# Performance work log

Hardware: AMD Instinct MI355X
Metric: run time of the kernel (lower is better)

The kernel has to match this reference:

```python
import jax, jax.numpy as jnp
import numpy as np

B, T, N, H = 256, 128, 512, 512
LB, UB = 0.0, 0.1
MAX_IT = 32  # bounded substitute for the data-dependent while loop (converges in a few iters)


def setup_inputs() -> dict:
    key = jax.random.key(0)
    ks = jax.random.split(key, 11)
    s = 1.0 / np.sqrt(H)
    u = lambda k, shape: jax.random.uniform(k, shape, jnp.float32, -s, s)
    return {
        "x": jax.random.normal(ks[0], (B, T, N), jnp.float32),
        "W_ih0": u(ks[1], (3 * H, N)), "W_hh0": u(ks[2], (3 * H, H)),
        "b_ih0": u(ks[3], (3 * H,)), "b_hh0": u(ks[4], (3 * H,)),
        "W_ih1": u(ks[5], (3 * H, H)), "W_hh1": u(ks[6], (3 * H, H)),
        "b_ih1": u(ks[7], (3 * H,)), "b_hh1": u(ks[8], (3 * H,)),
        "fc_w": u(ks[9], (N, H)), "fc_b": u(ks[10], (N,)),
    }


def gru_layer(x, W_ih, W_hh, b_ih, b_hh):
    # x: [B, T, I] -> hidden sequence [B, T, H]; matches torch.nn.GRU gate math.
    xi = jnp.einsum('bti,gi->btg', x, W_ih) + b_ih  # precompute input proj [B,T,3H]

    def step(h, xi_t):
        gh = h @ W_hh.T + b_hh
        xr, xz, xn = jnp.split(xi_t, 3, axis=-1)
        hr, hz, hn = jnp.split(gh, 3, axis=-1)
        r = jax.nn.sigmoid(xr + hr)
        z = jax.nn.sigmoid(xz + hz)
        n = jnp.tanh(xn + r * hn)
        h2 = (1.0 - z) * n + z * h
        return h2, h2

    h0 = jnp.zeros((x.shape[0], H), x.dtype)
    _, hs = jax.lax.scan(step, h0, jnp.swapaxes(xi, 0, 1))
    return jnp.swapaxes(hs, 0, 1)


def rebalance(w):
    # Water-filling: clamp to [LB, UB], redistribute clipped mass to non-capped
    # names proportionally, repeat until no weight exceeds UB. Bounded iteration
    # count with masked no-op updates (do-while semantics: body runs at least once).
    wc0 = jnp.clip(w, LB, UB)

    def body(st, _):
        old, wc, cont = st
        leftover = jnp.sum(old - wc)
        mask = wc != UB
        noms = jnp.where(mask, wc, 0.0)
        gift = leftover * noms / jnp.sum(noms)
        wc2 = wc + gift                      # gift is 0 where mask is False
        again = jnp.any(wc2 > UB)
        wc_next = jnp.where(again, jnp.clip(wc2, LB, UB), wc2)
        old_n = jnp.where(cont, wc2, old)
        wc_n = jnp.where(cont, wc_next, wc)
        return (old_n, wc_n, jnp.logical_and(cont, again)), None

    (old, wc, _), _ = jax.lax.scan(body, (w, wc0, jnp.array(True)), None, length=MAX_IT)
    return wc


def reference(x, W_ih0, W_hh0, b_ih0, b_hh0, W_ih1, W_hh1, b_ih1, b_hh1, fc_w, fc_b):
    h = gru_layer(x, W_ih0, W_hh0, b_ih0, b_hh0)
    h = gru_layer(h, W_ih1, W_hh1, b_ih1, b_hh1)
    h_t = h[:, -1, :]                        # last timestep [B, H]
    logit = h_t @ fc_w.T + fc_b              # dropout is identity in eval
    logit = jax.nn.softmax(jax.nn.silu(logit), axis=-1)
    return jax.vmap(rebalance)(logit)
```

## Files before the change

### kernel.cpp

```cpp
#include <hip/hip_runtime.h>
#include <math.h>

#define BB 256
#define TT 128
#define NN 512
#define HH 512
#define G3 1536
#define SLAB (HH * BB)
#define XSLAB (G3 * BB)
#define CH 16

typedef __attribute__((ext_vector_type(8))) short bf16x8;
typedef __attribute__((ext_vector_type(4))) float f32x4;

__device__ __forceinline__ unsigned short bf16_rne(float f) {
    union { float f; unsigned int u; } v; v.f = f;
    unsigned int r = (v.u + 0x7fffu + ((v.u >> 16) & 1u)) >> 16;
    return (unsigned short)r;
}
__device__ __forceinline__ float bf16_tof(unsigned short h) {
    union { float f; unsigned int u; } v; v.u = ((unsigned int)h) << 16;
    return v.f;
}
__device__ __forceinline__ float sigm(float v) { return 1.f / (1.f + expf(-v)); }

__global__ void zero_kernel(float* p, int n) {
    int i = blockIdx.x * blockDim.x + threadIdx.x;
    if (i < n) p[i] = 0.f;
}

__global__ __launch_bounds__(256) void convert_split(
    const float* __restrict__ in, unsigned short* __restrict__ hi,
    unsigned short* __restrict__ lo, int n) {
    int i = (blockIdx.x * 256 + threadIdx.x) * 4;
    if (i >= n) return;
    float4 v = *(const float4*)(in + i);
    float f[4] = {v.x, v.y, v.z, v.w};
    ushort4 h, l;
    unsigned short* hp = (unsigned short*)&h;
    unsigned short* lp = (unsigned short*)&l;
#pragma unroll
    for (int q = 0; q < 4; ++q) {
        unsigned short hh = bf16_rne(f[q]);
        hp[q] = hh;
        lp[q] = bf16_rne(f[q] - bf16_tof(hh));
    }
    *(ushort4*)(hi + i) = h;
    *(ushort4*)(lo + i) = l;
}

__global__ __launch_bounds__(128) void pack_rec(
    const float* __restrict__ Whh0, const float* __restrict__ Wih1,
    const float* __restrict__ Whh1, unsigned short* __restrict__ pk) {
    int bi = blockIdx.x;
    int set = bi >> 9, rem = bi & 511;
    int p = rem >> 4, kc = rem & 15;
    const float* W = (set == 0) ? Whh0 : (set == 1) ? Wih1 : Whh1;
    unsigned short* tp = pk + (size_t)bi * 4096;
    int tid = threadIdx.x;
#pragma unroll
    for (int i = 0; i < 12; ++i) {
        int idx = tid * 12 + i;
        int row = idx >> 5, k = idx & 31;
        int grow = (row >> 4) * 512 + p * 16 + (row & 15);
        float v = W[(size_t)grow * 512 + kc * 32 + k];
        unsigned short h = bf16_rne(v);
        tp[row * 40 + k] = h;
        tp[1920 + row * 40 + k] = bf16_rne(v - bf16_tof(h));
    }
    if (tid < 32)
#pragma unroll
        for (int i = 0; i < 8; ++i) tp[3840 + tid * 8 + i] = 0;
}

__global__ __launch_bounds__(256) void xi_mfma_x(
    const unsigned short* __restrict__ Wh, const unsigned short* __restrict__ Wl,
    const float* __restrict__ x, int t0,
    const float* __restrict__ bias, float* __restrict__ out) {
    __shared__ unsigned short As[2][128][40];
    __shared__ unsigned short Bs[2][128][40];
    const int tid = threadIdx.x;
    const int n0 = blockIdx.x * 128;
    const int g0 = blockIdx.y * 128;
    const int tl = n0 >> 8, b0 = n0 & 255;
    const int tg = t0 + tl;
    const int w = tid >> 6, lane = tid & 63;
    const int wg = (w >> 1) * 64, wb = (w & 1) * 64;
    const int l15 = lane & 15, l4 = lane >> 4;
    const int sr = tid >> 2, sc = (tid & 3) * 8;

    f32x4 acc[4][4] = {};
    for (int kc = 0; kc < 512; kc += 32) {
        uint4 a0 = *(const uint4*)(Wh + (size_t)(g0 + sr) * 512 + kc + sc);
        uint4 a1 = *(const uint4*)(Wh + (size_t)(g0 + 64 + sr) * 512 + kc + sc);
        uint4 a2 = *(const uint4*)(Wl + (size_t)(g0 + sr) * 512 + kc + sc);
        uint4 a3 = *(const uint4*)(Wl + (size_t)(g0 + 64 + sr) * 512 + kc + sc);
        const float* xr0 = x + ((size_t)(b0 + sr) * TT + tg) * NN + kc + sc;
        const float* xr1 = x + ((size_t)(b0 + 64 + sr) * TT + tg) * NN + kc + sc;
        float4 f00 = *(const float4*)xr0, f01 = *(const float4*)(xr0 + 4);
        float4 f10 = *(const float4*)xr1, f11 = *(const float4*)(xr1 + 4);
        float fa[8] = {f00.x, f00.y, f00.z, f00.w, f01.x, f01.y, f01.z, f01.w};
        float fb[8] = {f10.x, f10.y, f10.z, f10.w, f11.x, f11.y, f11.z, f11.w};
        unsigned short h0v[8], l0v[8], h1v[8], l1v[8];
#pragma unroll
        for (int q = 0; q < 8; ++q) {
            unsigned short hh = bf16_rne(fa[q]);
            h0v[q] = hh; l0v[q] = bf16_rne(fa[q] - bf16_tof(hh));
            hh = bf16_rne(fb[q]);
            h1v[q] = hh; l1v[q] = bf16_rne(fb[q] - bf16_tof(hh));
        }
        __syncthreads();
        *(uint4*)&As[0][sr][sc] = a0;      *(uint4*)&As[0][64 + sr][sc] = a1;
        *(uint4*)&As[1][sr][sc] = a2;      *(uint4*)&As[1][64 + sr][sc] = a3;
        *(uint4*)&Bs[0][sr][sc] = *(uint4*)h0v;  *(uint4*)&Bs[0][64 + sr][sc] = *(uint4*)h1v;
        *(uint4*)&Bs[1][sr][sc] = *(uint4*)l0v;  *(uint4*)&Bs[1][64 + sr][sc] = *(uint4*)l1v;
        __syncthreads();
        bf16x8 ah[4], al[4], bh[4], bl[4];
#pragma unroll
        for (int i = 0; i < 4; ++i) {
            ah[i] = *(const bf16x8*)&As[0][wg + 16 * i + l15][l4 * 8];
            al[i] = *(const bf16x8*)&As[1][wg + 16 * i + l15][l4 * 8];
            bh[i] = *(const bf16x8*)&Bs[0][wb + 16 * i + l15][l4 * 8];
            bl[i] = *(const bf16x8*)&Bs[1][wb + 16 * i + l15][l4 * 8];
        }
#pragma unroll
        for (int i = 0; i < 4; ++i)
#pragma unroll
            for (int j = 0; j < 4; ++j) {
                acc[i][j] = __builtin_amdgcn_mfma_f32_16x16x32_bf16(ah[i], bh[j], acc[i][j], 0, 0, 0);
                acc[i][j] = __builtin_amdgcn_mfma_f32_16x16x32_bf16(ah[i], bl[j], acc[i][j], 0, 0, 0);
                acc[i][j] = __builtin_amdgcn_mfma_f32_16x16x32_bf16(al[i], bh[j], acc[i][j], 0, 0, 0);
            }
    }
    float* op = out + (size_t)tl * XSLAB;
#pragma unroll
    for (int i = 0; i < 4; ++i) {
        int gbase = g0 + wg + 16 * i + l4 * 4;
#pragma unroll
        for (int r = 0; r < 4; ++r) {
            float bv = bias[gbase + r];
#pragma unroll
            for (int j = 0; j < 4; ++j)
                op[(size_t)(gbase + r) * 256 + b0 + wb + 16 * j + l15] = acc[i][j][r] + bv;
        }
    }
}

__global__ __launch_bounds__(256) void step_mfma(
    int s, const unsigned short* __restrict__ pk,
    const float* __restrict__ xi0, float* __restrict__ xi1,
    const float* __restrict__ bih1,
    const float* __restrict__ bhh0, const float* __restrict__ bhh1,
    float* __restrict__ h0f, float* __restrict__ h1f,
    unsigned short* __restrict__ H0h, unsigned short* __restrict__ H0l,
    unsigned short* __restrict__ H1h, unsigned short* __restrict__ H1l) {
    __shared__ __align__(16) unsigned short lds[16384];
    __shared__ float hs[16][33];
    const int bi = blockIdx.x;
    const int sec = bi >> 8;
    const int local = bi & 255;
    const int t = (sec == 0) ? s : (sec == 1) ? s - 1 : s - 2;
    if (t < 0 || t > 127) return;
    const int p = (local & 7) * 4 + ((local >> 3) & 3);
    const int bt = local >> 5;
    const int b0 = bt * 32;
    const int tid = threadIdx.x, w = tid >> 6, lane = tid & 63;
    const int l15 = lane & 15, l4 = lane >> 4;
    const int kk = w >> 1, bcol = w & 1;
    const int lt = tid & 127;

    const unsigned short *Bh, *Bl;
    if (sec == 0) { int sl = (t - 1) & 1; Bh = H0h + (size_t)sl * SLAB; Bl = H0l + (size_t)sl * SLAB; }
    else if (sec == 1) { int sl = t & 1; Bh = H0h + (size_t)sl * SLAB; Bl = H0l + (size_t)sl * SLAB; }
    else { int sl = (t - 1) & 1; Bh = H1h + (size_t)sl * SLAB; Bl = H1l + (size_t)sl * SLAB; }

    const unsigned short* Ab = pk + ((size_t)(sec * 32 + p) * 16) * 4096;
    const int brow = b0 + bcol * 16 + l15;
    const unsigned short* bhp = Bh + (size_t)brow * 512 + kk * 256 + l4 * 8;
    const unsigned short* blp = Bl + (size_t)brow * 512 + kk * 256 + l4 * 8;

    f32x4 cR = {0, 0, 0, 0}, cZ = cR, cN = cR;
    uint4 rg0, rg1, rg2, rg3;
    {
        const uint4* g0p = (const uint4*)Ab + (size_t)(kk * 8) * 256 + lt;
        rg0 = g0p[0]; rg1 = g0p[128];
        rg2 = g0p[0];
    }
    {
        const uint4* g0p = (const uint4*)Ab + (size_t)(kk * 8) * 512 + lt;
        rg0 = g0p[0]; rg1 = g0p[128]; rg2 = g0p[256]; rg3 = g0p[384];
        uint4* lp = (uint4*)lds + (kk * 2 + 0) * 512 + lt;
        lp[0] = rg0; lp[128] = rg1; lp[256] = rg2; lp[384] = rg3;
    }
    __syncthreads();
#pragma unroll
    for (int i = 0; i < 8; ++i) {
        const int d = i & 1;
        if (i < 7) {
            const uint4* gn = (const uint4*)Ab + (size_t)(kk * 8 + i + 1) * 512 + lt;
            rg0 = gn[0]; rg1 = gn[128]; rg2 = gn[256]; rg3 = gn[384];
        }
        const unsigned short* tb = lds + (kk * 2 + d) * 4096;
        bf16x8 aRh = *(const bf16x8*)(tb + (l15) * 40 + l4 * 8);
        bf16x8 aRl = *(const bf16x8*)(tb + 1920 + (l15) * 40 + l4 * 8);
        bf16x8 aZh = *(const bf16x8*)(tb + (16 + l15) * 40 + l4 * 8);
        bf16x8 aZl = *(const bf16x8*)(tb + 1920 + (16 + l15) * 40 + l4 * 8);
        bf16x8 aNh = *(const bf16x8*)(tb + (32 + l15) * 40 + l4 * 8);
        bf16x8 aNl = *(const bf16x8*)(tb + 1920 + (32 + l15) * 40 + l4 * 8);
        bf16x8 bh = *(const bf16x8*)(bhp + i * 32);
        bf16x8 bl = *(const bf16x8*)(blp + i * 32);
        cR = __builtin_amdgcn_mfma_f32_16x16x32_bf16(aRh, bh, cR, 0, 0, 0);
        cR = __builtin_amdgcn_mfma_f32_16x16x32_bf16(aRh, bl, cR, 0, 0, 0);
        cR = __builtin_amdgcn_mfma_f32_16x16x32_bf16(aRl, bh, cR, 0, 0, 0);
        cZ = __builtin_amdgcn_mfma_f32_16x16x32_bf16(aZh, bh, cZ, 0, 0, 0);
        cZ = __builtin_amdgcn_mfma_f32_16x16x32_bf16(aZh, bl, cZ, 0, 0, 0);
        cZ = __builtin_amdgcn_mfma_f32_16x16x32_bf16(aZl, bh, cZ, 0, 0, 0);
        cN = __builtin_amdgcn_mfma_f32_16x16x32_bf16(aNh, bh, cN, 0, 0, 0);
        cN = __builtin_amdgcn_mfma_f32_16x16x32_bf16(aNh, bl, cN, 0, 0, 0);
        cN = __builtin_amdgcn_mfma_f32_16x16x32_bf16(aNl, bh, cN, 0, 0, 0);
        if (i < 7) {
            uint4* lp = (uint4*)lds + (kk * 2 + (d ^ 1)) * 512 + lt;
            lp[0] = rg0; lp[128] = rg1; lp[256] = rg2; lp[384] = rg3;
        }
        __syncthreads();
    }
    float* red = (float*)lds;
    if (kk == 1) {
        int o = (bcol * 64 + lane) * 12;
        *(f32x4*)(red + o) = cR; *(f32x4*)(red + o + 4) = cZ; *(f32x4*)(red + o + 8) = cN;
    }
    __syncthreads();
    if (kk == 0) {
        int o = (bcol * 64 + lane) * 12;
        f32x4 u;
        u = *(f32x4*)(red + o);     cR += u;
        u = *(f32x4*)(red + o + 4); cZ += u;
        u = *(f32x4*)(red + o + 8); cN += u;
        const int b = b0 + bcol * 16 + l15;
        if (sec == 1) {
            float* xo = xi1 + (size_t)(t & 1) * XSLAB;
#pragma unroll
            for (int q = 0; q < 4; ++q) {
                int jrow = p * 16 + l4 * 4 + q;
                xo[(size_t)jrow * 256 + b]          = cR[q] + bih1[jrow];
                xo[(size_t)(512 + jrow) * 256 + b]  = cZ[q] + bih1[512 + jrow];
                xo[(size_t)(1024 + jrow) * 256 + b] = cN[q] + bih1[1024 + jrow];
            }
        } else {
            const float *xi, *bhh, *hpv;
            float* hnew;
            if (sec == 0) {
                xi = xi0 + (size_t)(t & (CH - 1)) * XSLAB;
                bhh = bhh0;
                hpv = h0f + (size_t)((t - 1) & 1) * SLAB;
                hnew = h0f + (size_t)(t & 1) * SLAB;
            } else {
                xi = xi1 + (size_t)(t & 1) * XSLAB;
                bhh = bhh1;
                hpv = h1f + (size_t)((t - 1) & 1) * SLAB;
                hnew = h1f + (size_t)(t & 1) * SLAB;
            }
#pragma unroll
            for (int q = 0; q < 4; ++q) {
                int jl = l4 * 4 + q;
                int jrow = p * 16 + jl;
                float xr = xi[(size_t)jrow * 256 + b];
                float xz = xi[(size_t)(512 + jrow) * 256 + b];
                float xn = xi[(size_t)(1024 + jrow) * 256 + b];
                float hp = hpv[(size_t)jrow * 256 + b];
                float rr = sigm(xr + cR[q] + bhh[jrow]);
                float zz = sigm(xz + cZ[q] + bhh[512 + jrow]);
                float nn = tanhf(xn + rr * (cN[q] + bhh[1024 + jrow]));
                float hv = (1.f - zz) * nn + zz * hp;
                hnew[(size_t)jrow * 256 + b] = hv;
                hs[jl][bcol * 16 + l15] = hv;
            }
        }
    }
    if (sec != 1) {
        __syncthreads();
        if (tid < 128) {
            int blocal = tid >> 2, j4 = (tid & 3) * 4;
            unsigned short hq[4], lq[4];
#pragma unroll
            for (int i2 = 0; i2 < 4; ++i2) {
                float v = hs[j4 + i2][blocal];
                unsigned short hh = bf16_rne(v);
                hq[i2] = hh; lq[i2] = bf16_rne(v - bf16_tof(hh));
            }
            unsigned short *Hh, *Hl;
            if (sec == 0) { Hh = H0h + (size_t)(t & 1) * SLAB; Hl = H0l + (size_t)(t & 1) * SLAB; }
            else          { Hh = H1h + (size_t)(t & 1) * SLAB; Hl = H1l + (size_t)(t & 1) * SLAB; }
            size_t o = (size_t)(b0 + blocal) * 512 + p * 16 + j4;
            *(ushort4*)(Hh + o) = *(ushort4*)hq;
            *(ushort4*)(Hl + o) = *(ushort4*)lq;
        }
    }
}


__global__ __launch_bounds__(256) void hT_to_h(
    const float* __restrict__ hT, float* __restrict__ h) {
    __shared__ float tb[64][65];
    const int tid = threadIdx.x;
    const int k0 = blockIdx.x * 64, b0 = blockIdx.y * 64;
#pragma unroll
    for (int i = 0; i < 4; ++i) {
        int r = (tid >> 4) + 16 * i;
        int c = (tid & 15) * 4;
        float4 v = *(const float4*)(hT + (size_t)(k0 + r) * 256 + b0 + c);
        tb[c + 0][r] = v.x; tb[c + 1][r] = v.y; tb[c + 2][r] = v.z; tb[c + 3][r] = v.w;
    }
    __syncthreads();
#pragma unroll
    for (int i = 0; i < 4; ++i) {
        int r = (tid >> 4) + 16 * i;
        int c = (tid & 15) * 4;
        float4 v;
        v.x = tb[r][c]; v.y = tb[r][c + 1]; v.z = tb[r][c + 2]; v.w = tb[r][c + 3];
        *(float4*)(h + (size_t)(b0 + r) * 512 + k0 + c) = v;
    }
}

__device__ __forceinline__ float blockReduceSum(float v, float* tmp) {
    __syncthreads();
#pragma unroll
    for (int o = 32; o; o >>= 1) v += __shfl_down(v, o);
    if ((threadIdx.x & 63) == 0) tmp[threadIdx.x >> 6] = v;
    __syncthreads();
    if (threadIdx.x == 0) tmp[4] = tmp[0] + tmp[1] + tmp[2] + tmp[3];
    __syncthreads();
    return tmp[4];
}

__device__ __forceinline__ float blockReduceMax(float v, float* tmp) {
    __syncthreads();
#pragma unroll
    for (int o = 32; o; o >>= 1) v = fmaxf(v, __shfl_down(v, o));
    if ((threadIdx.x & 63) == 0) tmp[threadIdx.x >> 6] = v;
    __syncthreads();
    if (threadIdx.x == 0) tmp[4] = fmaxf(fmaxf(tmp[0], tmp[1]), fmaxf(tmp[2], tmp[3]));
    __syncthreads();
    return tmp[4];
}

__global__ __launch_bounds__(256) void head_kernel(
    const float* __restrict__ h1, const float* __restrict__ fcw,
    const float* __restrict__ fcb, float* __restrict__ out) {
    __shared__ __align__(16) float hrow[512];
    __shared__ float wv[512];
    __shared__ float ov[512];
    __shared__ float tmp[8];
    const int b = blockIdx.x, tid = threadIdx.x;
    hrow[tid]       = h1[(size_t)b * 512 + tid];
    hrow[tid + 256] = h1[(size_t)b * 512 + 256 + tid];
    __syncthreads();

    float s[2];
#pragma unroll
    for (int q = 0; q < 2; ++q) {
        int n = tid + q * 256;
        const float* wr = fcw + (size_t)n * 512;
        float acc = 0.f;
        for (int k = 0; k < 512; k += 4) {
            float4 wq = *(const float4*)(wr + k);
            acc += wq.x * hrow[k] + wq.y * hrow[k + 1] + wq.z * hrow[k + 2] + wq.w * hrow[k + 3];
        }
        float l = acc + fcb[n];
        s[q] = l / (1.f + expf(-l));
    }

    float mx = blockReduceMax(fmaxf(s[0], s[1]), tmp);
    float e0 = expf(s[0] - mx), e1 = expf(s[1] - mx);
    float sum = blockReduceSum(e0 + e1, tmp);
    float w0 = e0 / sum, w1 = e1 / sum;

    ov[tid] = w0;       ov[tid + 256] = w1;
    wv[tid]       = fminf(fmaxf(w0, 0.f), 0.1f);
    wv[tid + 256] = fminf(fmaxf(w1, 0.f), 0.1f);
    __syncthreads();

    for (int it = 0; it < 32; ++it) {
        float wc0 = wv[tid], wc1 = wv[tid + 256];
        float o0 = ov[tid], o1 = ov[tid + 256];
        float leftover = blockReduceSum((o0 - wc0) + (o1 - wc1), tmp);
        float n0 = (wc0 != 0.1f) ? wc0 : 0.f;
        float n1 = (wc1 != 0.1f) ? wc1 : 0.f;
        float denom = blockReduceSum(n0 + n1, tmp);
        float w20 = wc0 + leftover * n0 / denom;
        float w21 = wc1 + leftover * n1 / denom;
        float fl = ((w20 > 0.1f) || (w21 > 0.1f)) ? 1.f : 0.f;
        bool again = blockReduceSum(fl, tmp) > 0.f;
        __syncthreads();
        ov[tid] = w20; ov[tid + 256] = w21;
        wv[tid]       = again ? fminf(fmaxf(w20, 0.f), 0.1f) : w20;
        wv[tid + 256] = again ? fminf(fmaxf(w21, 0.f), 0.1f) : w21;
        __syncthreads();
        if (!again) break;
    }

    out[(size_t)b * 512 + tid]       = wv[tid];
    out[(size_t)b * 512 + 256 + tid] = wv[tid + 256];
}

extern "C" void kernel_launch(void* const* d_in, const int* in_sizes, int n_in,
                              void* d_out, int out_size, void* d_ws, size_t ws_size,
                              hipStream_t stream) {
    const float* x    = (const float*)d_in[0];
    const float* Wih0 = (const float*)d_in[1];
    const float* Whh0 = (const float*)d_in[2];
    const float* bih0 = (const float*)d_in[3];
    const float* bhh0 = (const float*)d_in[4];
    const float* Wih1 = (const float*)d_in[5];
    const float* Whh1 = (const float*)d_in[6];
    const float* bih1 = (const float*)d_in[7];
    const float* bhh1 = (const float*)d_in[8];
    const float* fcw  = (const float*)d_in[9];
    const float* fcb  = (const float*)d_in[10];
    float* out = (float*)d_out;

    const size_t WHALF = (size_t)G3 * HH;
    unsigned short* W0h = (unsigned short*)d_ws;
    unsigned short* W0l = W0h + WHALF;
    unsigned short* pk  = W0l + WHALF;
    float* xi0 = (float*)(pk + (size_t)1536 * 4096);
    float* xi1 = xi0 + (size_t)CH * XSLAB;
    float* h0f = xi1 + 2 * (size_t)XSLAB;
    float* h1f = h0f + 2 * (size_t)SLAB;
    float* h1n = h1f + 2 * (size_t)SLAB;
    unsigned short* H0h = (unsigned short*)(h1n + SLAB);
    unsigned short* H0l = H0h + 2 * (size_t)SLAB;
    unsigned short* H1h = H0l + 2 * (size_t)SLAB;
    unsigned short* H1l = H1h + 2 * (size_t)SLAB;

    convert_split<<<(G3 * HH) / 1024, 256, 0, stream>>>(Wih0, W0h, W0l, G3 * HH);
    pack_rec<<<1536, 128, 0, stream>>>(Whh0, Wih1, Whh1, pk);
    zero_kernel<<<SLAB / 256, 256, 0, stream>>>(h0f + SLAB, SLAB);
    zero_kernel<<<SLAB / 256, 256, 0, stream>>>(h1f + SLAB, SLAB);
    zero_kernel<<<(SLAB / 2) / 256, 256, 0, stream>>>((float*)(H0h + SLAB), SLAB / 2);
    zero_kernel<<<(SLAB / 2) / 256, 256, 0, stream>>>((float*)(H0l + SLAB), SLAB / 2);
    zero_kernel<<<(SLAB / 2) / 256, 256, 0, stream>>>((float*)(H1h + SLAB), SLAB / 2);
    zero_kernel<<<(SLAB / 2) / 256, 256, 0, stream>>>((float*)(H1l + SLAB), SLAB / 2);

    for (int c = 0; c < TT / CH; ++c) {
        xi_mfma_x<<<dim3(CH * 2, 12), 256, 0, stream>>>(W0h, W0l, x, c * CH, bih0, xi0);
        for (int tl = 0; tl < CH; ++tl) {
            int s = c * CH + tl;
            step_mfma<<<768, 256, 0, stream>>>(s, pk, xi0, xi1, bih1, bhh0, bhh1,
                                               h0f, h1f, H0h, H0l, H1h, H1l);
        }
    }
    step_mfma<<<768, 256, 0, stream>>>(128, pk, xi0, xi1, bih1, bhh0, bhh1,
                                       h0f, h1f, H0h, H0l, H1h, H1l);
    step_mfma<<<768, 256, 0, stream>>>(129, pk, xi0, xi1, bih1, bhh0, bhh1,
                                       h0f, h1f, H0h, H0l, H1h, H1l);

    hT_to_h<<<dim3(8, 4), 256, 0, stream>>>(h1f + SLAB, h1n);
    head_kernel<<<BB, 256, 0, stream>>>(h1n, fcw, fcb, out);
}
```

Before: 2.100 ms.

## Pre-swizzle recurrent weights into MFMA fragment order and split K across 8 waves

```diff
diff --git a/kernel.cpp b/kernel.cpp
--- a/kernel.cpp
+++ b/kernel.cpp
@@ -12,14 +12,15 @@
 
 typedef __attribute__((ext_vector_type(8))) short bf16x8;
 typedef __attribute__((ext_vector_type(4))) float f32x4;
-
-__device__ __forceinline__ unsigned short bf16_rne(float f) {
-    union { float f; unsigned int u; } v; v.f = f;
-    unsigned int r = (v.u + 0x7fffu + ((v.u >> 16) & 1u)) >> 16;
-    return (unsigned short)r;
-}
-__device__ __forceinline__ float bf16_tof(unsigned short h) {
-    union { float f; unsigned int u; } v; v.u = ((unsigned int)h) << 16;
+typedef unsigned short ushort;
+
+__device__ __forceinline__ ushort bf16_rne(float f) {
+    union { float f; unsigned u; } v; v.f = f;
+    unsigned r = (v.u + 0x7fffu + ((v.u >> 16) & 1u)) >> 16;
+    return (ushort)r;
+}
+__device__ __forceinline__ float bf16_tof(ushort h) {
+    union { float f; unsigned u; } v; v.u = ((unsigned)h) << 16;
     return v.f;
 }
 __device__ __forceinline__ float sigm(float v) { return 1.f / (1.f + expf(-v)); }
@@ -30,55 +31,55 @@
 }
 
 __global__ __launch_bounds__(256) void convert_split(
-    const float* __restrict__ in, unsigned short* __restrict__ hi,
-    unsigned short* __restrict__ lo, int n) {
+    const float* __restrict__ in, ushort* __restrict__ hi,
+    ushort* __restrict__ lo, int n) {
     int i = (blockIdx.x * 256 + threadIdx.x) * 4;
     if (i >= n) return;
     float4 v = *(const float4*)(in + i);
     float f[4] = {v.x, v.y, v.z, v.w};
-    ushort4 h, l;
-    unsigned short* hp = (unsigned short*)&h;
-    unsigned short* lp = (unsigned short*)&l;
+    ushort h[4], l[4];
 #pragma unroll
     for (int q = 0; q < 4; ++q) {
-        unsigned short hh = bf16_rne(f[q]);
-        hp[q] = hh;
-        lp[q] = bf16_rne(f[q] - bf16_tof(hh));
-    }
-    *(ushort4*)(hi + i) = h;
-    *(ushort4*)(lo + i) = l;
-}
-
-__global__ __launch_bounds__(128) void pack_rec(
+        ushort hh = bf16_rne(f[q]);
+        h[q] = hh;
+        l[q] = bf16_rne(f[q] - bf16_tof(hh));
+    }
+    *(ushort4*)(hi + i) = *(ushort4*)h;
+    *(ushort4*)(lo + i) = *(ushort4*)l;
+}
+
+__global__ __launch_bounds__(64) void pack_swz(
     const float* __restrict__ Whh0, const float* __restrict__ Wih1,
-    const float* __restrict__ Whh1, unsigned short* __restrict__ pk) {
-    int bi = blockIdx.x;
-    int set = bi >> 9, rem = bi & 511;
-    int p = rem >> 4, kc = rem & 15;
-    const float* W = (set == 0) ? Whh0 : (set == 1) ? Wih1 : Whh1;
-    unsigned short* tp = pk + (size_t)bi * 4096;
-    int tid = threadIdx.x;
-#pragma unroll
-    for (int i = 0; i < 12; ++i) {
-        int idx = tid * 12 + i;
-        int row = idx >> 5, k = idx & 31;
-        int grow = (row >> 4) * 512 + p * 16 + (row & 15);
-        float v = W[(size_t)grow * 512 + kc * 32 + k];
-        unsigned short h = bf16_rne(v);
-        tp[row * 40 + k] = h;
-        tp[1920 + row * 40 + k] = bf16_rne(v - bf16_tof(h));
-    }
-    if (tid < 32)
-#pragma unroll
-        for (int i = 0; i < 8; ++i) tp[3840 + tid * 8 + i] = 0;
+    const float* __restrict__ Whh1, ushort* __restrict__ pk) {
+    const int bi = blockIdx.x;
+    const int it = bi & 3, kq = (bi >> 2) & 3, p = (bi >> 4) & 31, sec = bi >> 9;
+    const float* W = (sec == 0) ? Whh0 : (sec == 1) ? Wih1 : Whh1;
+    const int lane = threadIdx.x;
+    const int l15 = lane & 15, l4 = lane >> 4;
+    ushort* base = pk + (size_t)bi * 3072 + lane * 8;
+#pragma unroll
+    for (int g = 0; g < 3; ++g) {
+        int grow = g * 512 + p * 16 + l15;
+        const float* src = W + (size_t)grow * 512 + kq * 128 + it * 32 + l4 * 8;
+        ushort hs[8], ls[8];
+#pragma unroll
+        for (int e = 0; e < 8; ++e) {
+            float v = src[e];
+            ushort h = bf16_rne(v);
+            hs[e] = h;
+            ls[e] = bf16_rne(v - bf16_tof(h));
+        }
+        *(uint4*)(base + g * 1024) = *(uint4*)hs;
+        *(uint4*)(base + g * 1024 + 512) = *(uint4*)ls;
+    }
 }
 
 __global__ __launch_bounds__(256) void xi_mfma_x(
-    const unsigned short* __restrict__ Wh, const unsigned short* __restrict__ Wl,
+    const ushort* __restrict__ Wh, const ushort* __restrict__ Wl,
     const float* __restrict__ x, int t0,
     const float* __restrict__ bias, float* __restrict__ out) {
-    __shared__ unsigned short As[2][128][40];
-    __shared__ unsigned short Bs[2][128][40];
+    __shared__ ushort As[2][128][40];
+    __shared__ ushort Bs[2][128][40];
     const int tid = threadIdx.x;
     const int n0 = blockIdx.x * 128;
     const int g0 = blockIdx.y * 128;
@@ -101,10 +102,10 @@
         float4 f10 = *(const float4*)xr1, f11 = *(const float4*)(xr1 + 4);
         float fa[8] = {f00.x, f00.y, f00.z, f00.w, f01.x, f01.y, f01.z, f01.w};
         float fb[8] = {f10.x, f10.y, f10.z, f10.w, f11.x, f11.y, f11.z, f11.w};
-        unsigned short h0v[8], l0v[8], h1v[8], l1v[8];
+        ushort h0v[8], l0v[8], h1v[8], l1v[8];
 #pragma unroll
         for (int q = 0; q < 8; ++q) {
-            unsigned short hh = bf16_rne(fa[q]);
+            ushort hh = bf16_rne(fa[q]);
             h0v[q] = hh; l0v[q] = bf16_rne(fa[q] - bf16_tof(hh));
             hh = bf16_rne(fb[q]);
             h1v[q] = hh; l1v[q] = bf16_rne(fb[q] - bf16_tof(hh));
@@ -146,155 +147,142 @@
     }
 }
 
-__global__ __launch_bounds__(256) void step_mfma(
-    int s, const unsigned short* __restrict__ pk,
+__device__ __forceinline__ void kreduce(float* scr, int kq, int ct, int l15, int l4,
+                                        f32x4 acc[3]) {
+    const int slot = (kq >> 1) * 2 + ct;
+    const int pos0 = (l4 * 4) * 17 + l15;
+    __syncthreads();
+    if (kq & 1) {
+#pragma unroll
+        for (int g = 0; g < 3; ++g)
+#pragma unroll
+            for (int q = 0; q < 4; ++q)
+                scr[slot * 816 + g * 272 + pos0 + q * 17] = acc[g][q];
+    }
+    __syncthreads();
+    if (!(kq & 1)) {
+#pragma unroll
+        for (int g = 0; g < 3; ++g)
+#pragma unroll
+            for (int q = 0; q < 4; ++q)
+                acc[g][q] += scr[slot * 816 + g * 272 + pos0 + q * 17];
+    }
+    if (kq == 2) {
+#pragma unroll
+        for (int g = 0; g < 3; ++g)
+#pragma unroll
+            for (int q = 0; q < 4; ++q)
+                scr[(2 + ct) * 816 + g * 272 + pos0 + q * 17] = acc[g][q];
+    }
+    __syncthreads();
+    if (kq == 0) {
+#pragma unroll
+        for (int g = 0; g < 3; ++g)
+#pragma unroll
+            for (int q = 0; q < 4; ++q)
+                acc[g][q] += scr[(2 + ct) * 816 + g * 272 + pos0 + q * 17];
+    }
+}
+
+__device__ __forceinline__ void epi_xi(float* __restrict__ xo,
+    const float* __restrict__ bias, int p, int b0, int kq, int ct, int l15, int l4,
+    const f32x4 acc[3]) {
+    if (kq != 0) return;
+    const int b = b0 + ct * 16 + l15;
+#pragma unroll
+    for (int g = 0; g < 3; ++g)
+#pragma unroll
+        for (int q = 0; q < 4; ++q) {
+            int grow = g * 512 + p * 16 + l4 * 4 + q;
+            xo[(size_t)grow * 256 + b] = acc[g][q] + bias[grow];
+        }
+}
+
+__device__ __forceinline__ void epi_gru(const float* __restrict__ xi,
+    const float* __restrict__ bhh, const float* __restrict__ hpv,
+    float* __restrict__ hnew, ushort* __restrict__ Hh, ushort* __restrict__ Hl,
+    int p, int b0, int kq, int ct, int l15, int l4, const f32x4 acc[3]) {
+    if (kq != 0) return;
+    const int b = b0 + ct * 16 + l15;
+    ushort hq[4], lq[4];
+#pragma unroll
+    for (int q = 0; q < 4; ++q) {
+        int jrow = p * 16 + l4 * 4 + q;
+        float xr = xi[(size_t)jrow * 256 + b];
+        float xz = xi[(size_t)(512 + jrow) * 256 + b];
+        float xn = xi[(size_t)(1024 + jrow) * 256 + b];
+        float hp = hpv[(size_t)jrow * 256 + b];
+        float rr = sigm(xr + acc[0][q] + bhh[jrow]);
+        float zz = sigm(xz + acc[1][q] + bhh[512 + jrow]);
+        float nn = tanhf(xn + rr * (acc[2][q] + bhh[1024 + jrow]));
+        float hv = (1.f - zz) * nn + zz * hp;
+        hnew[(size_t)jrow * 256 + b] = hv;
+        ushort hh = bf16_rne(hv);
+        hq[q] = hh;
+        lq[q] = bf16_rne(hv - bf16_tof(hh));
+    }
+    size_t o = (size_t)b * 512 + p * 16 + l4 * 4;
+    *(ushort4*)(Hh + o) = *(ushort4*)hq;
+    *(ushort4*)(Hl + o) = *(ushort4*)lq;
+}
+
+__global__ __launch_bounds__(512) void step_v10(
+    int s, const ushort* __restrict__ pk,
     const float* __restrict__ xi0, float* __restrict__ xi1,
     const float* __restrict__ bih1,
     const float* __restrict__ bhh0, const float* __restrict__ bhh1,
     float* __restrict__ h0f, float* __restrict__ h1f,
-    unsigned short* __restrict__ H0h, unsigned short* __restrict__ H0l,
-    unsigned short* __restrict__ H1h, unsigned short* __restrict__ H1l) {
-    __shared__ __align__(16) unsigned short lds[16384];
-    __shared__ float hs[16][33];
+    ushort* __restrict__ H0h, ushort* __restrict__ H0l,
+    ushort* __restrict__ H1h, ushort* __restrict__ H1l) {
+    __shared__ float scr[3264];
     const int bi = blockIdx.x;
-    const int sec = bi >> 8;
-    const int local = bi & 255;
+    const int sec = bi >> 8, local = bi & 255;
     const int t = (sec == 0) ? s : (sec == 1) ? s - 1 : s - 2;
     if (t < 0 || t > 127) return;
     const int p = (local & 7) * 4 + ((local >> 3) & 3);
-    const int bt = local >> 5;
-    const int b0 = bt * 32;
+    const int b0 = (local >> 5) * 32;
     const int tid = threadIdx.x, w = tid >> 6, lane = tid & 63;
     const int l15 = lane & 15, l4 = lane >> 4;
-    const int kk = w >> 1, bcol = w & 1;
-    const int lt = tid & 127;
-
-    const unsigned short *Bh, *Bl;
-    if (sec == 0) { int sl = (t - 1) & 1; Bh = H0h + (size_t)sl * SLAB; Bl = H0l + (size_t)sl * SLAB; }
-    else if (sec == 1) { int sl = t & 1; Bh = H0h + (size_t)sl * SLAB; Bl = H0l + (size_t)sl * SLAB; }
-    else { int sl = (t - 1) & 1; Bh = H1h + (size_t)sl * SLAB; Bl = H1l + (size_t)sl * SLAB; }
-
-    const unsigned short* Ab = pk + ((size_t)(sec * 32 + p) * 16) * 4096;
-    const int brow = b0 + bcol * 16 + l15;
-    const unsigned short* bhp = Bh + (size_t)brow * 512 + kk * 256 + l4 * 8;
-    const unsigned short* blp = Bl + (size_t)brow * 512 + kk * 256 + l4 * 8;
-
-    f32x4 cR = {0, 0, 0, 0}, cZ = cR, cN = cR;
-    uint4 rg0, rg1, rg2, rg3;
-    {
-        const uint4* g0p = (const uint4*)Ab + (size_t)(kk * 8) * 256 + lt;
-        rg0 = g0p[0]; rg1 = g0p[128];
-        rg2 = g0p[0];
-    }
-    {
-        const uint4* g0p = (const uint4*)Ab + (size_t)(kk * 8) * 512 + lt;
-        rg0 = g0p[0]; rg1 = g0p[128]; rg2 = g0p[256]; rg3 = g0p[384];
-        uint4* lp = (uint4*)lds + (kk * 2 + 0) * 512 + lt;
-        lp[0] = rg0; lp[128] = rg1; lp[256] = rg2; lp[384] = rg3;
-    }
-    __syncthreads();
-#pragma unroll
-    for (int i = 0; i < 8; ++i) {
-        const int d = i & 1;
-        if (i < 7) {
-            const uint4* gn = (const uint4*)Ab + (size_t)(kk * 8 + i + 1) * 512 + lt;
-            rg0 = gn[0]; rg1 = gn[128]; rg2 = gn[256]; rg3 = gn[384];
-        }
-        const unsigned short* tb = lds + (kk * 2 + d) * 4096;
-        bf16x8 aRh = *(const bf16x8*)(tb + (l15) * 40 + l4 * 8);
-        bf16x8 aRl = *(const bf16x8*)(tb + 1920 + (l15) * 40 + l4 * 8);
-        bf16x8 aZh = *(const bf16x8*)(tb + (16 + l15) * 40 + l4 * 8);
-        bf16x8 aZl = *(const bf16x8*)(tb + 1920 + (16 + l15) * 40 + l4 * 8);
-        bf16x8 aNh = *(const bf16x8*)(tb + (32 + l15) * 40 + l4 * 8);
-        bf16x8 aNl = *(const bf16x8*)(tb + 1920 + (32 + l15) * 40 + l4 * 8);
-        bf16x8 bh = *(const bf16x8*)(bhp + i * 32);
-        bf16x8 bl = *(const bf16x8*)(blp + i * 32);
-        cR = __builtin_amdgcn_mfma_f32_16x16x32_bf16(aRh, bh, cR, 0, 0, 0);
-        cR = __builtin_amdgcn_mfma_f32_16x16x32_bf16(aRh, bl, cR, 0, 0, 0);
-        cR = __builtin_amdgcn_mfma_f32_16x16x32_bf16(aRl, bh, cR, 0, 0, 0);
-        cZ = __builtin_amdgcn_mfma_f32_16x16x32_bf16(aZh, bh, cZ, 0, 0, 0);
-        cZ = __builtin_amdgcn_mfma_f32_16x16x32_bf16(aZh, bl, cZ, 0, 0, 0);
-        cZ = __builtin_amdgcn_mfma_f32_16x16x32_bf16(aZl, bh, cZ, 0, 0, 0);
-        cN = __builtin_amdgcn_mfma_f32_16x16x32_bf16(aNh, bh, cN, 0, 0, 0);
-        cN = __builtin_amdgcn_mfma_f32_16x16x32_bf16(aNh, bl, cN, 0, 0, 0);
-        cN = __builtin_amdgcn_mfma_f32_16x16x32_bf16(aNl, bh, cN, 0, 0, 0);
-        if (i < 7) {
-            uint4* lp = (uint4*)lds + (kk * 2 + (d ^ 1)) * 512 + lt;
-            lp[0] = rg0; lp[128] = rg1; lp[256] = rg2; lp[384] = rg3;
-        }
-        __syncthreads();
-    }
-    float* red = (float*)lds;
-    if (kk == 1) {
-        int o = (bcol * 64 + lane) * 12;
-        *(f32x4*)(red + o) = cR; *(f32x4*)(red + o + 4) = cZ; *(f32x4*)(red + o + 8) = cN;
-    }
-    __syncthreads();
-    if (kk == 0) {
-        int o = (bcol * 64 + lane) * 12;
-        f32x4 u;
-        u = *(f32x4*)(red + o);     cR += u;
-        u = *(f32x4*)(red + o + 4); cZ += u;
-        u = *(f32x4*)(red + o + 8); cN += u;
-        const int b = b0 + bcol * 16 + l15;
-        if (sec == 1) {
-            float* xo = xi1 + (size_t)(t & 1) * XSLAB;
-#pragma unroll
-            for (int q = 0; q < 4; ++q) {
-                int jrow = p * 16 + l4 * 4 + q;
-                xo[(size_t)jrow * 256 + b]          = cR[q] + bih1[jrow];
-                xo[(size_t)(512 + jrow) * 256 + b]  = cZ[q] + bih1[512 + jrow];
-                xo[(size_t)(1024 + jrow) * 256 + b] = cN[q] + bih1[1024 + jrow];
-            }
-        } else {
-            const float *xi, *bhh, *hpv;
-            float* hnew;
-            if (sec == 0) {
-                xi = xi0 + (size_t)(t & (CH - 1)) * XSLAB;
-                bhh = bhh0;
-                hpv = h0f + (size_t)((t - 1) & 1) * SLAB;
-                hnew = h0f + (size_t)(t & 1) * SLAB;
-            } else {
-                xi = xi1 + (size_t)(t & 1) * XSLAB;
-                bhh = bhh1;
-                hpv = h1f + (size_t)((t - 1) & 1) * SLAB;
-                hnew = h1f + (size_t)(t & 1) * SLAB;
-            }
-#pragma unroll
-            for (int q = 0; q < 4; ++q) {
-                int jl = l4 * 4 + q;
-                int jrow = p * 16 + jl;
-                float xr = xi[(size_t)jrow * 256 + b];
-                float xz = xi[(size_t)(512 + jrow) * 256 + b];
-                float xn = xi[(size_t)(1024 + jrow) * 256 + b];
-                float hp = hpv[(size_t)jrow * 256 + b];
-                float rr = sigm(xr + cR[q] + bhh[jrow]);
-                float zz = sigm(xz + cZ[q] + bhh[512 + jrow]);
-                float nn = tanhf(xn + rr * (cN[q] + bhh[1024 + jrow]));
-                float hv = (1.f - zz) * nn + zz * hp;
-                hnew[(size_t)jrow * 256 + b] = hv;
-                hs[jl][bcol * 16 + l15] = hv;
-            }
-        }
-    }
-    if (sec != 1) {
-        __syncthreads();
-        if (tid < 128) {
-            int blocal = tid >> 2, j4 = (tid & 3) * 4;
-            unsigned short hq[4], lq[4];
-#pragma unroll
-            for (int i2 = 0; i2 < 4; ++i2) {
-                float v = hs[j4 + i2][blocal];
-                unsigned short hh = bf16_rne(v);
-                hq[i2] = hh; lq[i2] = bf16_rne(v - bf16_tof(hh));
-            }
-            unsigned short *Hh, *Hl;
-            if (sec == 0) { Hh = H0h + (size_t)(t & 1) * SLAB; Hl = H0l + (size_t)(t & 1) * SLAB; }
-            else          { Hh = H1h + (size_t)(t & 1) * SLAB; Hl = H1l + (size_t)(t & 1) * SLAB; }
-            size_t o = (size_t)(b0 + blocal) * 512 + p * 16 + j4;
-            *(ushort4*)(Hh + o) = *(ushort4*)hq;
-            *(ushort4*)(Hl + o) = *(ushort4*)lq;
-        }
+    const int kq = w >> 1, ct = w & 1;
+
+    const ushort *Bh, *Bl;
+    if (sec == 0)      { int sl = (t - 1) & 1; Bh = H0h + (size_t)sl * SLAB; Bl = H0l + (size_t)sl * SLAB; }
+    else if (sec == 1) { int sl = t & 1;       Bh = H0h + (size_t)sl * SLAB; Bl = H0l + (size_t)sl * SLAB; }
+    else               { int sl = (t - 1) & 1; Bh = H1h + (size_t)sl * SLAB; Bl = H1l + (size_t)sl * SLAB; }
+
+    const ushort* baseA = pk + (size_t)((sec * 32 + p) * 4 + kq) * 12288 + lane * 8;
+    const int brow = b0 + ct * 16 + l15;
+    const ushort* bhp = Bh + (size_t)brow * 512 + kq * 128 + l4 * 8;
+    const ushort* blp = Bl + (size_t)brow * 512 + kq * 128 + l4 * 8;
+
+    f32x4 acc[3] = {};
+#pragma unroll
+    for (int it = 0; it < 4; ++it) {
+        bf16x8 bh = *(const bf16x8*)(bhp + it * 32);
+        bf16x8 bl = *(const bf16x8*)(blp + it * 32);
+#pragma unroll
+        for (int g = 0; g < 3; ++g) {
+            const ushort* rec = baseA + (it * 3 + g) * 1024;
+            bf16x8 ah = *(const bf16x8*)rec;
+            bf16x8 al = *(const bf16x8*)(rec + 512);
+            acc[g] = __builtin_amdgcn_mfma_f32_16x16x32_bf16(ah, bh, acc[g], 0, 0, 0);
+            acc[g] = __builtin_amdgcn_mfma_f32_16x16x32_bf16(ah, bl, acc[g], 0, 0, 0);
+            acc[g] = __builtin_amdgcn_mfma_f32_16x16x32_bf16(al, bh, acc[g], 0, 0, 0);
+        }
+    }
+    kreduce(scr, kq, ct, l15, l4, acc);
+    if (sec == 1) {
+        epi_xi(xi1 + (size_t)(t & 1) * XSLAB, bih1, p, b0, kq, ct, l15, l4, acc);
+    } else if (sec == 0) {
+        epi_gru(xi0 + (size_t)(t & (CH - 1)) * XSLAB, bhh0,
+                h0f + (size_t)((t - 1) & 1) * SLAB, h0f + (size_t)(t & 1) * SLAB,
+                H0h + (size_t)(t & 1) * SLAB, H0l + (size_t)(t & 1) * SLAB,
+                p, b0, kq, ct, l15, l4, acc);
+    } else {
+        epi_gru(xi1 + (size_t)(t & 1) * XSLAB, bhh1,
+                h1f + (size_t)((t - 1) & 1) * SLAB, h1f + (size_t)(t & 1) * SLAB,
+                H1h + (size_t)(t & 1) * SLAB, H1l + (size_t)(t & 1) * SLAB,
+                p, b0, kq, ct, l15, l4, acc);
     }
 }
 
@@ -306,16 +294,14 @@
     const int k0 = blockIdx.x * 64, b0 = blockIdx.y * 64;
 #pragma unroll
     for (int i = 0; i < 4; ++i) {
-        int r = (tid >> 4) + 16 * i;
-        int c = (tid & 15) * 4;
+        int r = (tid >> 4) + 16 * i, c = (tid & 15) * 4;
         float4 v = *(const float4*)(hT + (size_t)(k0 + r) * 256 + b0 + c);
         tb[c + 0][r] = v.x; tb[c + 1][r] = v.y; tb[c + 2][r] = v.z; tb[c + 3][r] = v.w;
     }
     __syncthreads();
 #pragma unroll
     for (int i = 0; i < 4; ++i) {
-        int r = (tid >> 4) + 16 * i;
-        int c = (tid & 15) * 4;
+        int r = (tid >> 4) + 16 * i, c = (tid & 15) * 4;
         float4 v;
         v.x = tb[r][c]; v.y = tb[r][c + 1]; v.z = tb[r][c + 2]; v.w = tb[r][c + 3];
         *(float4*)(h + (size_t)(b0 + r) * 512 + k0 + c) = v;
@@ -420,21 +406,21 @@
     float* out = (float*)d_out;
 
     const size_t WHALF = (size_t)G3 * HH;
-    unsigned short* W0h = (unsigned short*)d_ws;
-    unsigned short* W0l = W0h + WHALF;
-    unsigned short* pk  = W0l + WHALF;
-    float* xi0 = (float*)(pk + (size_t)1536 * 4096);
+    ushort* W0h = (ushort*)d_ws;
+    ushort* W0l = W0h + WHALF;
+    ushort* pk  = W0l + WHALF;
+    float* xi0 = (float*)(pk + (size_t)1536 * 3072);
     float* xi1 = xi0 + (size_t)CH * XSLAB;
     float* h0f = xi1 + 2 * (size_t)XSLAB;
     float* h1f = h0f + 2 * (size_t)SLAB;
     float* h1n = h1f + 2 * (size_t)SLAB;
-    unsigned short* H0h = (unsigned short*)(h1n + SLAB);
-    unsigned short* H0l = H0h + 2 * (size_t)SLAB;
-    unsigned short* H1h = H0l + 2 * (size_t)SLAB;
-    unsigned short* H1l = H1h + 2 * (size_t)SLAB;
+    ushort* H0h = (ushort*)(h1n + SLAB);
+    ushort* H0l = H0h + 2 * (size_t)SLAB;
+    ushort* H1h = H0l + 2 * (size_t)SLAB;
+    ushort* H1l = H1h + 2 * (size_t)SLAB;
 
     convert_split<<<(G3 * HH) / 1024, 256, 0, stream>>>(Wih0, W0h, W0l, G3 * HH);
-    pack_rec<<<1536, 128, 0, stream>>>(Whh0, Wih1, Whh1, pk);
+    pack_swz<<<1536, 64, 0, stream>>>(Whh0, Wih1, Whh1, pk);
     zero_kernel<<<SLAB / 256, 256, 0, stream>>>(h0f + SLAB, SLAB);
     zero_kernel<<<SLAB / 256, 256, 0, stream>>>(h1f + SLAB, SLAB);
     zero_kernel<<<(SLAB / 2) / 256, 256, 0, stream>>>((float*)(H0h + SLAB), SLAB / 2);
@@ -446,14 +432,14 @@
         xi_mfma_x<<<dim3(CH * 2, 12), 256, 0, stream>>>(W0h, W0l, x, c * CH, bih0, xi0);
         for (int tl = 0; tl < CH; ++tl) {
             int s = c * CH + tl;
-            step_mfma<<<768, 256, 0, stream>>>(s, pk, xi0, xi1, bih1, bhh0, bhh1,
-                                               h0f, h1f, H0h, H0l, H1h, H1l);
-        }
-    }
-    step_mfma<<<768, 256, 0, stream>>>(128, pk, xi0, xi1, bih1, bhh0, bhh1,
-                                       h0f, h1f, H0h, H0l, H1h, H1l);
-    step_mfma<<<768, 256, 0, stream>>>(129, pk, xi0, xi1, bih1, bhh0, bhh1,
-                                       h0f, h1f, H0h, H0l, H1h, H1l);
+            step_v10<<<768, 512, 0, stream>>>(s, pk, xi0, xi1, bih1, bhh0, bhh1,
+                                              h0f, h1f, H0h, H0l, H1h, H1l);
+        }
+    }
+    step_v10<<<768, 512, 0, stream>>>(128, pk, xi0, xi1, bih1, bhh0, bhh1,
+                                      h0f, h1f, H0h, H0l, H1h, H1l);
+    step_v10<<<768, 512, 0, stream>>>(129, pk, xi0, xi1, bih1, bhh0, bhh1,
+                                      h0f, h1f, H0h, H0l, H1h, H1l);
 
     hT_to_h<<<dim3(8, 4), 256, 0, stream>>>(h1f + SLAB, h1n);
     head_kernel<<<BB, 256, 0, stream>>>(h1n, fcw, fcb, out);
```

New measurement: 2.165 ms. 3.1% more time.
